# Performance work log

Hardware: AMD Instinct MI355X
Metric: run time of the kernel (lower is better)

Reference implementation:

```python
import jax, jax.numpy as jnp
import numpy as np

N, M, G, H, ND, E = 4096, 8192, 8, 128, 16, 131072
MAX_PERIOD = 10000.0


def setup_inputs() -> dict:
    key = jax.random.key(0)
    ks = jax.random.split(key, 24)
    s = 0.05
    inp = {
        "x": jax.random.normal(ks[0], (N, ND), jnp.float32),
        "edge_index": jax.random.randint(ks[1], (2, E), 0, N),
        "timestep": jax.random.randint(ks[2], (G,), 0, 1000),
        "batch_map": jnp.sort(jax.random.randint(ks[3], (N,), 0, G)),
        "obj_nucleotide_mask": jax.random.randint(ks[4], (M,), 0, 3),
        "obj_central_mask": jax.random.bernoulli(ks[5], 0.3, (M,)),
        "obj_backbone_mask": jax.random.bernoulli(ks[6], 0.5, (M,)),
        "obj_x": jax.random.normal(ks[7], (M, ND - 3), jnp.float32),
        "obj_pos": jax.random.normal(ks[8], (M, 3), jnp.float32),
        "obj_batch": jnp.sort(jax.random.randint(ks[9], (M,), 0, G)),
        # params (stored [in, out]; y = x @ W + b)
        "W_node": s * jax.random.normal(ks[10], (ND, H)),
        "b_node": jnp.zeros((H,)),
        "W_cond": s * jax.random.normal(ks[11], (H, H)),
        "b_cond": jnp.zeros((H,)),
        "W_time": s * jax.random.normal(ks[12], (H, H)),
        "b_time": jnp.zeros((H,)),
        "W_conv1": s * jax.random.normal(ks[13], (H, H)),
        "b_conv1": jnp.zeros((H,)),
        "W_conv2": s * jax.random.normal(ks[14], (H, H)),
        "b_conv2": jnp.zeros((H,)),
        "W_out": s * jax.random.normal(ks[15], (H, ND)),
        "b_out": jnp.zeros((ND,)),
        "w_edge": s * jax.random.normal(ks[16], (2 * H,)),
        "b_edge": jnp.zeros(()),
    }
    return inp


def timestep_embedding(t, dim):
    half = dim // 2
    freqs = jnp.exp(-np.log(MAX_PERIOD) * jnp.arange(half, dtype=jnp.float32) / half)
    args = t[:, None].astype(jnp.float32) * freqs[None]
    return jnp.concatenate([jnp.cos(args), jnp.sin(args)], axis=-1)


def gcn_conv(xh, src, dst, norm, W, b, n):
    # x' = D^-1/2 (A+I) D^-1/2 (X W) + b  (PyG GCNConv, self-loops included in src/dst/norm)
    xw = xh @ W
    msg = xw[src] * norm[:, None]
    return jax.ops.segment_sum(msg, dst, num_segments=n) + b


def reference(x, edge_index, timestep, batch_map, obj_nucleotide_mask,
              obj_central_mask, obj_backbone_mask, obj_x, obj_pos, obj_batch,
              W_node, b_node, W_cond, b_cond, W_time, b_time,
              W_conv1, b_conv1, W_conv2, b_conv2, W_out, b_out, w_edge, b_edge):
    n = x.shape[0]
    # timestep embedding + projections
    time_emb = timestep_embedding(timestep, H)            # [G, H]
    node_emb = x @ W_node + b_node                        # [N, H]

    # condition node pooling (masked mean per graph)
    is_left = obj_nucleotide_mask == 0
    is_central = obj_central_mask
    is_right = obj_nucleotide_mask == 2
    is_base = ~obj_backbone_mask
    is_cond = is_left | (is_central & is_base) | (is_right & is_base)  # [M]
    cond_x = jnp.concatenate([obj_x, obj_pos], axis=1)    # [M, ND]
    cond_emb = cond_x @ W_node + b_node                   # [M, H]
    cm = is_cond.astype(cond_emb.dtype)
    sums = jax.ops.segment_sum(cond_emb * cm[:, None], obj_batch, num_segments=G)
    cnt = jax.ops.segment_sum(cm, obj_batch, num_segments=G)
    pooled = sums / jnp.maximum(cnt, 1.0)[:, None]        # [G, H]

    time_h = time_emb @ W_time + b_time                   # [G, H]
    cond_h = pooled @ W_cond + b_cond                     # [G, H]
    node_emb = node_emb + time_h[batch_map] + cond_h[batch_map]

    # GCN normalization with self-loops (shared by both conv layers)
    loop = jnp.arange(n)
    src = jnp.concatenate([edge_index[0], loop])
    dst = jnp.concatenate([edge_index[1], loop])
    deg = jax.ops.segment_sum(jnp.ones_like(src, jnp.float32), dst, num_segments=n)
    dinv = jnp.where(deg > 0, jax.lax.rsqrt(jnp.maximum(deg, 1.0)), 0.0)
    norm = dinv[src] * dinv[dst]

    h = jax.nn.relu(gcn_conv(node_emb, src, dst, norm, W_conv1, b_conv1, n))
    h = jax.nn.relu(gcn_conv(h, src, dst, norm, W_conv2, b_conv2, n))

    node_noise_pred = h @ W_out + b_out                   # [N, ND]

    # all-pairs edge logits: cat([h[row], h[col]]) @ w_edge + b
    # == (h @ w_left)[row] + (h @ w_right)[col] + b  (same math, avoids [P, 2H])
    row, col = jnp.triu_indices(n, k=1)
    s_l = h @ w_edge[:H]
    s_r = h @ w_edge[H:]
    edge_logits = s_l[row] + s_r[col] + b_edge            # [N*(N-1)/2]
    return (node_noise_pred, edge_logits)
```

## Files before the change

### kernel.cpp

```cpp
#include <hip/hip_runtime.h>

#define NN 4096
#define MM 8192
#define GG 8
#define HH 128
#define NDD 16
#define EE 131072
#define CBLK 64
#define COBJ (MM / CBLK)
#define HBLK 16
#define HEDGE (EE / HBLK)

typedef float nt_f4 __attribute__((ext_vector_type(4)));

__global__ __launch_bounds__(256) void k_front(
    const float* __restrict__ obj_x, const float* __restrict__ obj_pos,
    const int* __restrict__ nuc, const int* __restrict__ central,
    const int* __restrict__ backbone, const int* __restrict__ obj_batch,
    const int* __restrict__ e_dst, int* __restrict__ phist,
    float* __restrict__ partial, float* __restrict__ pcnt,
    const float* __restrict__ Wn, const float* __restrict__ Wc1,
    float* __restrict__ W1p) {
    int b = blockIdx.x, t = threadIdx.x;
    if (b < CBLK) {
        __shared__ float ls[GG * NDD];
        __shared__ float lc[GG];
        if (t < GG * NDD) ls[t] = 0.f;
        if (t < GG) lc[t] = 0.f;
        __syncthreads();
        int d = t & 15, oi = t >> 4;
        int base = b * COBJ;
#pragma unroll
        for (int pass = 0; pass < COBJ / 16; pass++) {
            int o = base + pass * 16 + oi;
            int nv = nuc[o];
            bool isb = (backbone[o] == 0);
            bool cond = (nv == 0) || ((central[o] != 0) && isb) || ((nv == 2) && isb);
            if (cond) {
                float v = (d < 13) ? obj_x[o * 13 + d] : obj_pos[o * 3 + (d - 13)];
                int g = obj_batch[o];
                atomicAdd(&ls[g * NDD + d], v);
                if (d == 0) atomicAdd(&lc[g], 1.f);
            }
        }
        __syncthreads();
        if (t < GG * NDD) partial[b * (GG * NDD) + t] = ls[t];
        if (t < GG) pcnt[b * GG + t] = lc[t];
        return;
    }
    if (b < CBLK + HBLK) {
        int hb = b - CBLK;
        __shared__ int hist[NN];
        for (int i = t; i < NN; i += 256) hist[i] = 0;
        __syncthreads();
        const int4* ed4 = ((const int4*)e_dst) + hb * (HEDGE / 4);
        for (int i = t; i < HEDGE / 4; i += 256) {
            int4 d4 = ed4[i];
            atomicAdd(&hist[d4.x], 1);
            atomicAdd(&hist[d4.y], 1);
            atomicAdd(&hist[d4.z], 1);
            atomicAdd(&hist[d4.w], 1);
        }
        __syncthreads();
        int4* ph4 = (int4*)(phist + hb * NN);
        for (int i = t; i < NN / 4; i += 256) ph4[i] = ((int4*)hist)[i];
        return;
    }
    int j = t & 127, a0 = t >> 7;
#pragma unroll
    for (int ai = 0; ai < 8; ai++) {
        int a = a0 + 2 * ai;
        float acc = 0.f;
        for (int k = 0; k < HH; k++) acc += Wn[a * HH + k] * Wc1[k * HH + j];
        W1p[a * HH + j] = acc;
    }
}

__global__ __launch_bounds__(1024) void k_mid(
    const int* __restrict__ timestep, const float* __restrict__ partial,
    const float* __restrict__ pcnt, const float* __restrict__ Wn,
    const float* __restrict__ bn, const float* __restrict__ Wt,
    const float* __restrict__ bt, const float* __restrict__ Wc,
    const float* __restrict__ bc, const float* __restrict__ Wc1,
    float* __restrict__ c1, const int* __restrict__ phist,
    int* __restrict__ row_ptr, int* __restrict__ cursor,
    float* __restrict__ dinv, const float* __restrict__ x,
    const float* __restrict__ W1p, float* __restrict__ xw) {
    int b = blockIdx.x, t = threadIdx.x;
    if (b == 0) {
        __shared__ float s16[GG * NDD];
        __shared__ float cinv[GG];
        __shared__ float te[GG * HH];
        __shared__ float pool[GG * HH];
        __shared__ float v2[GG * HH];
        int g = t >> 7, j = t & 127;
        if (t < GG * NDD) {
            float s = 0.f;
            for (int q = 0; q < CBLK; q++) s += partial[q * (GG * NDD) + t];
            s16[t] = s;
        }
        if (t < GG) {
            float c = 0.f;
            for (int q = 0; q < CBLK; q++) c += pcnt[q * GG + t];
            cinv[t] = 1.f / fmaxf(c, 1.f);
        }
        float tv = (float)timestep[g];
        float val;
        if (j < 64) {
            float f = expf(-logf(10000.f) * (float)j / 64.f);
            val = cosf(tv * f);
        } else {
            float f = expf(-logf(10000.f) * (float)(j - 64) / 64.f);
            val = sinf(tv * f);
        }
        te[t] = val;
        __syncthreads();
        float p = bn[j];
#pragma unroll
        for (int d = 0; d < NDD; d++) p += s16[g * NDD + d] * cinv[g] * Wn[d * HH + j];
        pool[t] = p;
        __syncthreads();
        float acc = bt[j] + bc[j] + bn[j];
        for (int k = 0; k < HH; k++) {
            acc += te[g * HH + k] * Wt[k * HH + j] + pool[g * HH + k] * Wc[k * HH + j];
        }
        v2[t] = acc;
        __syncthreads();
        float cc = 0.f;
        for (int k = 0; k < HH; k++) cc += v2[g * HH + k] * Wc1[k * HH + j];
        c1[t] = cc;
    } else if (b == 1) {
        __shared__ int aux[1024];
        int4 d4 = {0, 0, 0, 0};
        const int4* ph4 = (const int4*)phist;
#pragma unroll
        for (int h = 0; h < HBLK; h++) {
            int4 v = ph4[h * (NN / 4) + t];
            d4.x += v.x; d4.y += v.y; d4.z += v.z; d4.w += v.w;
        }
        int s = d4.x + d4.y + d4.z + d4.w;
        aux[t] = s;
        __syncthreads();
        for (int off = 1; off < 1024; off <<= 1) {
            int v = (t >= off) ? aux[t - off] : 0;
            __syncthreads();
            aux[t] += v;
            __syncthreads();
        }
        int run = (t > 0) ? aux[t - 1] : 0;
        int d[4] = {d4.x, d4.y, d4.z, d4.w};
#pragma unroll
        for (int i = 0; i < 4; i++) {
            int idx = t * 4 + i;
            row_ptr[idx] = run;
            cursor[idx] = run;
            dinv[idx] = rsqrtf((float)(d[i] + 1));
            run += d[i];
        }
        if (t == 1023) row_ptr[NN] = run;
    } else {
        __shared__ float xt[32 * NDD];
        int r0 = (b - 2) * 32;
        if (t < 512) xt[t] = x[r0 * NDD + t];
        __syncthreads();
        int col = t & 127, rh = t >> 7;
        float acc[4] = {0.f, 0.f, 0.f, 0.f};
#pragma unroll
        for (int k = 0; k < NDD; k++) {
            float w = W1p[k * HH + col];
#pragma unroll
            for (int i = 0; i < 4; i++) acc[i] += xt[(rh * 4 + i) * NDD + k] * w;
        }
#pragma unroll
        for (int i = 0; i < 4; i++) xw[(r0 + rh * 4 + i) * HH + col] = acc[i];
    }
}

__global__ __launch_bounds__(256) void k_scatfix(
    const int* __restrict__ e_src, const int* __restrict__ e_dst,
    int* __restrict__ cursor, int* __restrict__ col_idx,
    const float* __restrict__ c1, const int* __restrict__ bm,
    const float* __restrict__ dinv, float* __restrict__ xw) {
    int b = blockIdx.x, t = threadIdx.x;
    if (b < 128) {
        int i4 = b * 256 + t;
        int4 d4 = ((const int4*)e_dst)[i4];
        int4 s4 = ((const int4*)e_src)[i4];
        int p;
        p = atomicAdd(&cursor[d4.x], 1); col_idx[p] = s4.x;
        p = atomicAdd(&cursor[d4.y], 1); col_idx[p] = s4.y;
        p = atomicAdd(&cursor[d4.z], 1); col_idx[p] = s4.z;
        p = atomicAdd(&cursor[d4.w], 1); col_idx[p] = s4.w;
        return;
    }
    int r0 = (b - 128) * 8;
    int col = t & 127, rh = t >> 7;
#pragma unroll
    for (int i = 0; i < 4; i++) {
        int row = r0 + rh * 4 + i;
        xw[row * HH + col] = (xw[row * HH + col] + c1[bm[row] * HH + col]) * dinv[row];
    }
}

__global__ __launch_bounds__(256) void k_conv1(
    const float* __restrict__ xw, const int* __restrict__ row_ptr,
    const int* __restrict__ col_idx, const float* __restrict__ dinv,
    const float* __restrict__ b1, const float* __restrict__ Wc2,
    float* __restrict__ xw2) {
    int w = threadIdx.x >> 6, l = threadIdx.x & 63;
    int dst = blockIdx.x * 4 + w;
    const float2* xwp = (const float2*)xw;
    float2 acc = xwp[dst * 64 + l];
    int beg = row_ptr[dst], end = row_ptr[dst + 1];
    int e = beg;
    for (; e + 3 < end; e += 4) {
        int s0 = col_idx[e], s1 = col_idx[e + 1], s2 = col_idx[e + 2], s3 = col_idx[e + 3];
        float2 v0 = xwp[s0 * 64 + l], v1 = xwp[s1 * 64 + l];
        float2 v2 = xwp[s2 * 64 + l], v3 = xwp[s3 * 64 + l];
        acc.x += (v0.x + v1.x) + (v2.x + v3.x);
        acc.y += (v0.y + v1.y) + (v2.y + v3.y);
    }
    for (; e < end; e++) {
        float2 v = xwp[col_idx[e] * 64 + l];
        acc.x += v.x;
        acc.y += v.y;
    }
    float dd = dinv[dst];
    float2 h;
    h.x = fmaxf(dd * acc.x + b1[2 * l], 0.f);
    h.y = fmaxf(dd * acc.y + b1[2 * l + 1], 0.f);
    __shared__ float hr[4][HH];
    *(float2*)&hr[w][2 * l] = h;
    __syncthreads();
    float2 o = {0.f, 0.f};
#pragma unroll 4
    for (int k = 0; k < HH; k++) {
        float hk = hr[w][k];
        float2 wv = *(const float2*)&Wc2[k * HH + 2 * l];
        o.x += hk * wv.x;
        o.y += hk * wv.y;
    }
    o.x *= dd;
    o.y *= dd;
    ((float2*)xw2)[dst * 64 + l] = o;
}

__global__ __launch_bounds__(256) void k_conv2_head(
    const float* __restrict__ xw, const int* __restrict__ row_ptr,
    const int* __restrict__ col_idx, const float* __restrict__ dinv,
    const float* __restrict__ b2, const float* __restrict__ Wo,
    const float* __restrict__ bo, const float* __restrict__ we,
    float* __restrict__ out_pred, float* __restrict__ sl, float* __restrict__ sr) {
    int w = threadIdx.x >> 6, l = threadIdx.x & 63;
    int dst = blockIdx.x * 4 + w;
    const float2* xwp = (const float2*)xw;
    float2 acc = xwp[dst * 64 + l];
    int beg = row_ptr[dst], end = row_ptr[dst + 1];
    int e = beg;
    for (; e + 3 < end; e += 4) {
        int s0 = col_idx[e], s1 = col_idx[e + 1], s2 = col_idx[e + 2], s3 = col_idx[e + 3];
        float2 v0 = xwp[s0 * 64 + l], v1 = xwp[s1 * 64 + l];
        float2 v2 = xwp[s2 * 64 + l], v3 = xwp[s3 * 64 + l];
        acc.x += (v0.x + v1.x) + (v2.x + v3.x);
        acc.y += (v0.y + v1.y) + (v2.y + v3.y);
    }
    for (; e < end; e++) {
        float2 v = xwp[col_idx[e] * 64 + l];
        acc.x += v.x;
        acc.y += v.y;
    }
    float dd = dinv[dst];
    float2 h;
    h.x = fmaxf(dd * acc.x + b2[2 * l], 0.f);
    h.y = fmaxf(dd * acc.y + b2[2 * l + 1], 0.f);
    __shared__ float hr[4][HH];
    *(float2*)&hr[w][2 * l] = h;
    __syncthreads();
    {
        int c = l & 15, p = l >> 4;
        float a = 0.f;
#pragma unroll 4
        for (int k = p * 32; k < p * 32 + 32; k++) a += hr[w][k] * Wo[k * NDD + c];
        a += __shfl_xor(a, 16);
        a += __shfl_xor(a, 32);
        if (p == 0) out_pred[dst * NDD + c] = a + bo[c];
    }
    {
        float h0 = hr[w][l], h1v = hr[w][64 + l];
        float pl = h0 * we[l] + h1v * we[64 + l];
        float pr = h0 * we[HH + l] + h1v * we[HH + 64 + l];
        for (int off = 32; off; off >>= 1) {
            pl += __shfl_down(pl, off);
            pr += __shfl_down(pr, off);
        }
        if (l == 0) {
            sl[dst] = pl;
            sr[dst] = pr;
        }
    }
}

__global__ __launch_bounds__(256) void k_edges(const float* __restrict__ sl,
                                               const float* __restrict__ sr,
                                               const float* __restrict__ be_p,
                                               float* __restrict__ out) {
    int b = blockIdx.x, t = threadIdx.x;
    float be = be_p[0];
#pragma unroll
    for (int half = 0; half < 2; half++) {
        int r = half == 0 ? b : (NN - 2 - b);
        int off = r * (2 * NN - r - 1) / 2;
        int len = NN - 1 - r;
        float s = sl[r] + be;
        const float* sp = sr + r + 1;
        float* op = out + off;
        int hd = (4 - (off & 3)) & 3;
        if (hd > len) hd = len;
        if (t < hd) __builtin_nontemporal_store(s + sp[t], op + t);
        int body = (len - hd) >> 2;
        float* opb = op + hd;
        const float* spb = sp + hd;
        for (int i = t; i < body; i += 256) {
            int base = 4 * i;
            nt_f4 v;
            v.x = s + spb[base];
            v.y = s + spb[base + 1];
            v.z = s + spb[base + 2];
            v.w = s + spb[base + 3];
            __builtin_nontemporal_store(v, (nt_f4*)(opb + base));
        }
        int tail = hd + body * 4;
        int rem = len - tail;
        if (t < rem) __builtin_nontemporal_store(s + sp[tail + t], op + tail + t);
    }
}

extern "C" void kernel_launch(void* const* d_in, const int* in_sizes, int n_in,
                              void* d_out, int out_size, void* d_ws, size_t ws_size,
                              hipStream_t stream) {
    const float* x = (const float*)d_in[0];
    const int* e_src = (const int*)d_in[1];
    const int* e_dst = e_src + EE;
    const int* timestep = (const int*)d_in[2];
    const int* batch_map = (const int*)d_in[3];
    const int* nuc = (const int*)d_in[4];
    const int* central = (const int*)d_in[5];
    const int* backbone = (const int*)d_in[6];
    const float* obj_x = (const float*)d_in[7];
    const float* obj_pos = (const float*)d_in[8];
    const int* obj_batch = (const int*)d_in[9];
    const float* W_node = (const float*)d_in[10];
    const float* b_node = (const float*)d_in[11];
    const float* W_cond = (const float*)d_in[12];
    const float* b_cond = (const float*)d_in[13];
    const float* W_time = (const float*)d_in[14];
    const float* b_time = (const float*)d_in[15];
    const float* W_conv1 = (const float*)d_in[16];
    const float* b_conv1 = (const float*)d_in[17];
    const float* W_conv2 = (const float*)d_in[18];
    const float* b_conv2 = (const float*)d_in[19];
    const float* W_out = (const float*)d_in[20];
    const float* b_out = (const float*)d_in[21];
    const float* w_edge = (const float*)d_in[22];
    const float* b_edge = (const float*)d_in[23];

    float* ws = (float*)d_ws;
    float* bufA = ws;
    float* bufB = bufA + NN * HH;
    float* W1p = bufB + NN * HH;
    float* c1 = W1p + NDD * HH;
    float* partial = c1 + GG * HH;
    float* pcnt = partial + CBLK * GG * NDD;
    float* dinv = pcnt + CBLK * GG;
    float* sl = dinv + NN;
    float* sr = sl + NN;
    int* phist = (int*)(sr + NN);
    int* row_ptr = phist + HBLK * NN;
    int* cursor = row_ptr + NN + 1;
    int* col_idx = cursor + NN;

    float* out_pred = (float*)d_out;
    float* out_edges = out_pred + NN * NDD;

    k_front<<<CBLK + HBLK + 1, 256, 0, stream>>>(obj_x, obj_pos, nuc, central,
                                                 backbone, obj_batch, e_dst, phist,
                                                 partial, pcnt, W_node, W_conv1, W1p);
    k_mid<<<2 + NN / 32, 1024, 0, stream>>>(timestep, partial, pcnt, W_node, b_node,
                                            W_time, b_time, W_cond, b_cond, W_conv1,
                                            c1, phist, row_ptr, cursor, dinv, x, W1p,
                                            bufA);
    k_scatfix<<<128 + 512, 256, 0, stream>>>(e_src, e_dst, cursor, col_idx, c1,
                                             batch_map, dinv, bufA);
    k_conv1<<<NN / 4, 256, 0, stream>>>(bufA, row_ptr, col_idx, dinv, b_conv1,
                                        W_conv2, bufB);
    k_conv2_head<<<NN / 4, 256, 0, stream>>>(bufB, row_ptr, col_idx, dinv, b_conv2,
                                             W_out, b_out, w_edge, out_pred, sl, sr);
    k_edges<<<NN / 2, 256, 0, stream>>>(sl, sr, b_edge, out_edges);
}
```

Baseline: 204.9 us.

## Parallelize small GEMV stages across blocks, unroll gathers, stage Wc2 in LDS

Spreads the W_node·W_conv1 product over 8 blocks instead of one, and splits the per-graph conditioning chain across 8 blocks with a k-split reduction in shared memory. This shortens the serial single-block tails in the front kernels. The GCN neighbor gather loops gain an 8-way unrolled path to keep more loads in flight. The conv1 epilogue stages W_conv2 through 32KB of LDS in two halves, which adds barriers and LDS use that may reduce occupancy.

```diff
diff --git a/kernel.cpp b/kernel.cpp
--- a/kernel.cpp
+++ b/kernel.cpp
@@ -10,6 +10,7 @@
 #define COBJ (MM / CBLK)
 #define HBLK 16
 #define HEDGE (EE / HBLK)
+#define WBLK 8
 
 typedef float nt_f4 __attribute__((ext_vector_type(4)));
 
@@ -66,14 +67,12 @@
         for (int i = t; i < NN / 4; i += 256) ph4[i] = ((int4*)hist)[i];
         return;
     }
+    int wb = b - (CBLK + HBLK);
     int j = t & 127, a0 = t >> 7;
-#pragma unroll
-    for (int ai = 0; ai < 8; ai++) {
-        int a = a0 + 2 * ai;
-        float acc = 0.f;
-        for (int k = 0; k < HH; k++) acc += Wn[a * HH + k] * Wc1[k * HH + j];
-        W1p[a * HH + j] = acc;
-    }
+    int a = wb * 2 + a0;
+    float acc = 0.f;
+    for (int k = 0; k < HH; k++) acc += Wn[a * HH + k] * Wc1[k * HH + j];
+    W1p[a * HH + j] = acc;
 }
 
 __global__ __launch_bounds__(1024) void k_mid(
@@ -87,49 +86,70 @@
     float* __restrict__ dinv, const float* __restrict__ x,
     const float* __restrict__ W1p, float* __restrict__ xw) {
     int b = blockIdx.x, t = threadIdx.x;
-    if (b == 0) {
-        __shared__ float s16[GG * NDD];
-        __shared__ float cinv[GG];
-        __shared__ float te[GG * HH];
-        __shared__ float pool[GG * HH];
-        __shared__ float v2[GG * HH];
-        int g = t >> 7, j = t & 127;
-        if (t < GG * NDD) {
+    if (b < GG) {
+        int g = b;
+        __shared__ float s16[NDD];
+        __shared__ float te[HH];
+        __shared__ float pool[HH];
+        __shared__ float v2[HH];
+        __shared__ float vpart[8][HH];
+        __shared__ float cinv;
+        int j = t & 127, kq = t >> 7;
+        if (t < HH) {
+            float tv = (float)timestep[g];
+            float val;
+            if (t < 64) {
+                float f = expf(-logf(10000.f) * (float)t / 64.f);
+                val = cosf(tv * f);
+            } else {
+                float f = expf(-logf(10000.f) * (float)(t - 64) / 64.f);
+                val = sinf(tv * f);
+            }
+            te[t] = val;
+        } else if (t < HH + NDD) {
+            int d = t - HH;
             float s = 0.f;
-            for (int q = 0; q < CBLK; q++) s += partial[q * (GG * NDD) + t];
-            s16[t] = s;
-        }
-        if (t < GG) {
+            for (int q = 0; q < CBLK; q++) s += partial[q * (GG * NDD) + g * NDD + d];
+            s16[d] = s;
+        } else if (t == HH + NDD) {
             float c = 0.f;
-            for (int q = 0; q < CBLK; q++) c += pcnt[q * GG + t];
-            cinv[t] = 1.f / fmaxf(c, 1.f);
-        }
-        float tv = (float)timestep[g];
-        float val;
-        if (j < 64) {
-            float f = expf(-logf(10000.f) * (float)j / 64.f);
-            val = cosf(tv * f);
-        } else {
-            float f = expf(-logf(10000.f) * (float)(j - 64) / 64.f);
-            val = sinf(tv * f);
-        }
-        te[t] = val;
-        __syncthreads();
-        float p = bn[j];
-#pragma unroll
-        for (int d = 0; d < NDD; d++) p += s16[g * NDD + d] * cinv[g] * Wn[d * HH + j];
-        pool[t] = p;
-        __syncthreads();
-        float acc = bt[j] + bc[j] + bn[j];
-        for (int k = 0; k < HH; k++) {
-            acc += te[g * HH + k] * Wt[k * HH + j] + pool[g * HH + k] * Wc[k * HH + j];
-        }
-        v2[t] = acc;
-        __syncthreads();
-        float cc = 0.f;
-        for (int k = 0; k < HH; k++) cc += v2[g * HH + k] * Wc1[k * HH + j];
-        c1[t] = cc;
-    } else if (b == 1) {
+            for (int q = 0; q < CBLK; q++) c += pcnt[q * GG + g];
+            cinv = 1.f / fmaxf(c, 1.f);
+        }
+        __syncthreads();
+        if (t < HH) {
+            float p = bn[t];
+#pragma unroll
+            for (int d = 0; d < NDD; d++) p += s16[d] * cinv * Wn[d * HH + t];
+            pool[t] = p;
+        }
+        __syncthreads();
+        float acc = 0.f;
+#pragma unroll 4
+        for (int k = kq * 16; k < kq * 16 + 16; k++)
+            acc += te[k] * Wt[k * HH + j] + pool[k] * Wc[k * HH + j];
+        vpart[kq][j] = acc;
+        __syncthreads();
+        if (t < HH) {
+            float v = bt[t] + bc[t] + bn[t];
+#pragma unroll
+            for (int q = 0; q < 8; q++) v += vpart[q][t];
+            v2[t] = v;
+        }
+        __syncthreads();
+        acc = 0.f;
+#pragma unroll 4
+        for (int k = kq * 16; k < kq * 16 + 16; k++) acc += v2[k] * Wc1[k * HH + j];
+        __syncthreads();
+        vpart[kq][j] = acc;
+        __syncthreads();
+        if (t < HH) {
+            float c = 0.f;
+#pragma unroll
+            for (int q = 0; q < 8; q++) c += vpart[q][t];
+            c1[g * HH + t] = c;
+        }
+    } else if (b == GG) {
         __shared__ int aux[1024];
         int4 d4 = {0, 0, 0, 0};
         const int4* ph4 = (const int4*)phist;
@@ -160,7 +180,7 @@
         if (t == 1023) row_ptr[NN] = run;
     } else {
         __shared__ float xt[32 * NDD];
-        int r0 = (b - 2) * 32;
+        int r0 = (b - (GG + 1)) * 32;
         if (t < 512) xt[t] = x[r0 * NDD + t];
         __syncthreads();
         int col = t & 127, rh = t >> 7;
@@ -213,6 +233,16 @@
     float2 acc = xwp[dst * 64 + l];
     int beg = row_ptr[dst], end = row_ptr[dst + 1];
     int e = beg;
+    for (; e + 7 < end; e += 8) {
+        int s0 = col_idx[e], s1 = col_idx[e + 1], s2 = col_idx[e + 2], s3 = col_idx[e + 3];
+        int s4 = col_idx[e + 4], s5 = col_idx[e + 5], s6 = col_idx[e + 6], s7 = col_idx[e + 7];
+        float2 v0 = xwp[s0 * 64 + l], v1 = xwp[s1 * 64 + l];
+        float2 v2 = xwp[s2 * 64 + l], v3 = xwp[s3 * 64 + l];
+        float2 v4 = xwp[s4 * 64 + l], v5 = xwp[s5 * 64 + l];
+        float2 v6 = xwp[s6 * 64 + l], v7 = xwp[s7 * 64 + l];
+        acc.x += ((v0.x + v1.x) + (v2.x + v3.x)) + ((v4.x + v5.x) + (v6.x + v7.x));
+        acc.y += ((v0.y + v1.y) + (v2.y + v3.y)) + ((v4.y + v5.y) + (v6.y + v7.y));
+    }
     for (; e + 3 < end; e += 4) {
         int s0 = col_idx[e], s1 = col_idx[e + 1], s2 = col_idx[e + 2], s3 = col_idx[e + 3];
         float2 v0 = xwp[s0 * 64 + l], v1 = xwp[s1 * 64 + l];
@@ -230,15 +260,25 @@
     h.x = fmaxf(dd * acc.x + b1[2 * l], 0.f);
     h.y = fmaxf(dd * acc.y + b1[2 * l + 1], 0.f);
     __shared__ float hr[4][HH];
+    __shared__ float wsm[64 * HH];
     *(float2*)&hr[w][2 * l] = h;
-    __syncthreads();
     float2 o = {0.f, 0.f};
+#pragma unroll
+    for (int half = 0; half < 2; half++) {
+        __syncthreads();
+        const float4* src4 = (const float4*)(Wc2 + half * 64 * HH);
+        float4* dst4 = (float4*)wsm;
+#pragma unroll
+        for (int i = 0; i < (64 * HH / 4) / 256; i++)
+            dst4[i * 256 + threadIdx.x] = src4[i * 256 + threadIdx.x];
+        __syncthreads();
 #pragma unroll 4
-    for (int k = 0; k < HH; k++) {
-        float hk = hr[w][k];
-        float2 wv = *(const float2*)&Wc2[k * HH + 2 * l];
-        o.x += hk * wv.x;
-        o.y += hk * wv.y;
+        for (int k = 0; k < 64; k++) {
+            float hk = hr[w][half * 64 + k];
+            float2 wv = *(const float2*)&wsm[k * HH + 2 * l];
+            o.x += hk * wv.x;
+            o.y += hk * wv.y;
+        }
     }
     o.x *= dd;
     o.y *= dd;
@@ -257,6 +297,16 @@
     float2 acc = xwp[dst * 64 + l];
     int beg = row_ptr[dst], end = row_ptr[dst + 1];
     int e = beg;
+    for (; e + 7 < end; e += 8) {
+        int s0 = col_idx[e], s1 = col_idx[e + 1], s2 = col_idx[e + 2], s3 = col_idx[e + 3];
+        int s4 = col_idx[e + 4], s5 = col_idx[e + 5], s6 = col_idx[e + 6], s7 = col_idx[e + 7];
+        float2 v0 = xwp[s0 * 64 + l], v1 = xwp[s1 * 64 + l];
+        float2 v2 = xwp[s2 * 64 + l], v3 = xwp[s3 * 64 + l];
+        float2 v4 = xwp[s4 * 64 + l], v5 = xwp[s5 * 64 + l];
+        float2 v6 = xwp[s6 * 64 + l], v7 = xwp[s7 * 64 + l];
+        acc.x += ((v0.x + v1.x) + (v2.x + v3.x)) + ((v4.x + v5.x) + (v6.x + v7.x));
+        acc.y += ((v0.y + v1.y) + (v2.y + v3.y)) + ((v4.y + v5.y) + (v6.y + v7.y));
+    }
     for (; e + 3 < end; e += 4) {
         int s0 = col_idx[e], s1 = col_idx[e + 1], s2 = col_idx[e + 2], s3 = col_idx[e + 3];
         float2 v0 = xwp[s0 * 64 + l], v1 = xwp[s1 * 64 + l];
@@ -382,13 +432,13 @@
     float* out_pred = (float*)d_out;
     float* out_edges = out_pred + NN * NDD;
 
-    k_front<<<CBLK + HBLK + 1, 256, 0, stream>>>(obj_x, obj_pos, nuc, central,
-                                                 backbone, obj_batch, e_dst, phist,
-                                                 partial, pcnt, W_node, W_conv1, W1p);
-    k_mid<<<2 + NN / 32, 1024, 0, stream>>>(timestep, partial, pcnt, W_node, b_node,
-                                            W_time, b_time, W_cond, b_cond, W_conv1,
-                                            c1, phist, row_ptr, cursor, dinv, x, W1p,
-                                            bufA);
+    k_front<<<CBLK + HBLK + WBLK, 256, 0, stream>>>(obj_x, obj_pos, nuc, central,
+                                                    backbone, obj_batch, e_dst, phist,
+                                                    partial, pcnt, W_node, W_conv1, W1p);
+    k_mid<<<GG + 1 + NN / 32, 1024, 0, stream>>>(timestep, partial, pcnt, W_node,
+                                                 b_node, W_time, b_time, W_cond, b_cond,
+                                                 W_conv1, c1, phist, row_ptr, cursor,
+                                                 dinv, x, W1p, bufA);
     k_scatfix<<<128 + 512, 256, 0, stream>>>(e_src, e_dst, cursor, col_idx, c1,
                                              batch_map, dinv, bufA);
     k_conv1<<<NN / 4, 256, 0, stream>>>(bufA, row_ptr, col_idx, dinv, b_conv1,
```

New measurement: 170.9 us. 1.2x faster.
